# Kernel tuning notes

Hardware: AMD Instinct MI355X
Metric: run time of the kernel (lower is better)

Reference implementation:

```python
import jax, jax.numpy as jnp
import numpy as np

NUM_ITERS = 3  # num_iterations init arg


def squash(t, axis):
    # scale = ||t||^2 / (1+||t||^2); out = scale * t / ||t||
    sn = jnp.sum(t * t, axis=axis, keepdims=True)
    return (sn / (1.0 + sn)) * t / jnp.sqrt(sn)


def setup_inputs() -> dict:
    key = jax.random.key(0)
    k1, k2, k3 = jax.random.split(key, 3)
    B, I, O, DI, DO = 2048, 64, 32, 16, 16
    x = jax.random.normal(k1, (B, DI, I), dtype=jnp.float32)
    route_weights = jax.random.normal(k2, (O, I, DO, DI), dtype=jnp.float32)
    noise = 0.01 * jax.random.normal(k3, (O, I, DO, DI), dtype=jnp.float32)
    return {"x": x, "route_weights": route_weights, "noise": noise}


def reference(x, route_weights, noise):
    # random=True branch: perturbed routing weights
    W = route_weights + noise                      # [O,I,do,di]
    xt = jnp.transpose(x, (0, 2, 1))               # [B,I,di]
    # priors[b,o,i,d] = sum_e W[o,i,d,e] * xt[b,i,e]  (trailing singleton dim dropped)
    priors = jnp.einsum('oide,bie->boid', W, xt)   # [B,O,I,do]
    logits = jnp.zeros_like(priors)
    out = None
    for it in range(NUM_ITERS):
        probs = jax.nn.softmax(logits, axis=2)     # over input capsules I
        out = squash(jnp.sum(probs * priors, axis=2, keepdims=True), axis=3)  # [B,O,1,do]
        if it != NUM_ITERS - 1:
            logits = logits + priors * out         # routing-by-agreement update
    out = out[:, :, 0, :]                          # squeeze -> [B,O,do]
    # unsqueeze(0).transpose(2,1) -> [1,O,B,do]
    return jnp.transpose(out[None], (0, 2, 1, 3))
```

## Files before the change

kernel.cpp:

```cpp
#include <hip/hip_runtime.h>


#define THREADS 512

__global__ __launch_bounds__(THREADS) void routing_kernel(
    const float* __restrict__ x,
    const float* __restrict__ rw,
    const float* __restrict__ ns,
    float* __restrict__ out)
{
    __shared__ float lds[16384];

    const int tid  = threadIdx.x;
    const int w    = tid >> 6;
    const int lane = tid & 63;

    const int o  = blockIdx.x >> 6;
    const int bc = blockIdx.x & 63;
    const int bbase = bc * 32;

    float wq0[16], wq1[16];
    {
        const int base = (o * 64 + lane) * 256 + w * 32;
        #pragma unroll
        for (int eq = 0; eq < 4; ++eq) {
            const float4 a0 = *reinterpret_cast<const float4*>(rw + base + eq * 4);
            const float4 n0 = *reinterpret_cast<const float4*>(ns + base + eq * 4);
            wq0[4*eq+0] = a0.x + n0.x;  wq0[4*eq+1] = a0.y + n0.y;
            wq0[4*eq+2] = a0.z + n0.z;  wq0[4*eq+3] = a0.w + n0.w;
            const float4 a1 = *reinterpret_cast<const float4*>(rw + base + 16 + eq * 4);
            const float4 n1 = *reinterpret_cast<const float4*>(ns + base + 16 + eq * 4);
            wq1[4*eq+0] = a1.x + n1.x;  wq1[4*eq+1] = a1.y + n1.y;
            wq1[4*eq+2] = a1.z + n1.z;  wq1[4*eq+3] = a1.w + n1.w;
        }
    }

    const float* xrd = lds + 8192 + lane;
    const int d0 = 2 * w, d1 = 2 * w + 1;
    const int perm0 = ((((lane >> 2) ^ (d0 & 7)) << 2) | (lane & 3));
    const int perm1 = ((((lane >> 2) ^ (d1 & 7)) << 2) | (lane & 3));
    float* pw0 = lds + d0 * 64 + perm0;
    float* pw1 = lds + d1 * 64 + perm1;

    const int qB  = lane >> 4;
    const int dB  = lane & 15;
    const int swz = dB & 7;
    const float4* prbase = reinterpret_cast<const float4*>(lds) + (w * 16 + dB) * 16;
    const float4* pr0 = prbase + ((4 * qB + 0) ^ swz);
    const float4* pr1 = prbase + ((4 * qB + 1) ^ swz);
    const float4* pr2 = prbase + ((4 * qB + 2) ^ swz);
    const float4* pr3 = prbase + ((4 * qB + 3) ^ swz);

    float4* xwr = reinterpret_cast<float4*>(lds + 8192) + (w * 256 + lane);
    const float4* xsrc0 = reinterpret_cast<const float4*>(x) + bbase * 256
                        + (w * 256 + lane);

    const int outbase = (o * 2048 + bbase + w) * 16 + dB;

    float4 xb0 = xsrc0[0];
    float4 xb1 = xsrc0[64];
    float4 xb2 = xsrc0[128];
    float4 xb3 = xsrc0[192];
    xwr[0] = xb0;  xwr[64] = xb1;  xwr[128] = xb2;  xwr[192] = xb3;
    __syncthreads();

    #pragma unroll
    for (int s = 0; s < 4; ++s) {
        #pragma unroll
        for (int bb = 0; bb < 8; ++bb) {
            float xv[16];
            #pragma unroll
            for (int e = 0; e < 16; ++e)
                xv[e] = xrd[bb * 1024 + e * 64];
            float acc0 = 0.f, acc1 = 0.f;
            #pragma unroll
            for (int e = 0; e < 16; ++e) {
                acc0 = fmaf(wq0[e], xv[e], acc0);
                acc1 = fmaf(wq1[e], xv[e], acc1);
            }
            pw0[bb * 1024] = acc0;
            pw1[bb * 1024] = acc1;
        }
        __syncthreads();

        float p[16];
        {
            const float4 v0 = *pr0, v1 = *pr1, v2 = *pr2, v3 = *pr3;
            p[0]=v0.x; p[1]=v0.y; p[2]=v0.z; p[3]=v0.w;
            p[4]=v1.x; p[5]=v1.y; p[6]=v1.z; p[7]=v1.w;
            p[8]=v2.x; p[9]=v2.y; p[10]=v2.z; p[11]=v2.w;
            p[12]=v3.x; p[13]=v3.y; p[14]=v3.z; p[15]=v3.w;
        }

        if (s < 3) {
            const float4* xsrc = xsrc0 + (s + 1) * 2048;
            xb0 = xsrc[0];  xb1 = xsrc[64];  xb2 = xsrc[128];  xb3 = xsrc[192];
        }

        float t0 = (p[0]+p[1]) + (p[2]+p[3]);
        float t1 = (p[4]+p[5]) + (p[6]+p[7]);
        float t2 = (p[8]+p[9]) + (p[10]+p[11]);
        float t3 = (p[12]+p[13]) + (p[14]+p[15]);
        float part = (t0 + t1) + (t2 + t3);
        part += __shfl_xor(part, 16);
        part += __shfl_xor(part, 32);
        float sv = part * (1.0f / 64.0f);

        float sn = sv * sv;
        sn += __shfl_xor(sn, 1); sn += __shfl_xor(sn, 2);
        sn += __shfl_xor(sn, 4); sn += __shfl_xor(sn, 8);
        float factor = __builtin_amdgcn_sqrtf(sn)
                     * __builtin_amdgcn_rcpf(1.0f + sn);
        float Vsum = sv * factor;

        #pragma unroll
        for (int it = 0; it < 2; ++it) {
            const float c = Vsum * 1.44269504089f;
            float e0, e1, e2, e3;
            float dd0, dd1, dd2, dd3, nn0, nn1, nn2, nn3;
            e0 = __builtin_amdgcn_exp2f(p[0] * c);
            e1 = __builtin_amdgcn_exp2f(p[1] * c);
            e2 = __builtin_amdgcn_exp2f(p[2] * c);
            e3 = __builtin_amdgcn_exp2f(p[3] * c);
            dd0 = e0; dd1 = e1; dd2 = e2; dd3 = e3;
            nn0 = e0 * p[0]; nn1 = e1 * p[1]; nn2 = e2 * p[2]; nn3 = e3 * p[3];
            e0 = __builtin_amdgcn_exp2f(p[4] * c);
            e1 = __builtin_amdgcn_exp2f(p[5] * c);
            e2 = __builtin_amdgcn_exp2f(p[6] * c);
            e3 = __builtin_amdgcn_exp2f(p[7] * c);
            dd0 += e0; dd1 += e1; dd2 += e2; dd3 += e3;
            nn0 = fmaf(e0, p[4], nn0); nn1 = fmaf(e1, p[5], nn1);
            nn2 = fmaf(e2, p[6], nn2); nn3 = fmaf(e3, p[7], nn3);
            e0 = __builtin_amdgcn_exp2f(p[8] * c);
            e1 = __builtin_amdgcn_exp2f(p[9] * c);
            e2 = __builtin_amdgcn_exp2f(p[10] * c);
            e3 = __builtin_amdgcn_exp2f(p[11] * c);
            dd0 += e0; dd1 += e1; dd2 += e2; dd3 += e3;
            nn0 = fmaf(e0, p[8], nn0);  nn1 = fmaf(e1, p[9], nn1);
            nn2 = fmaf(e2, p[10], nn2); nn3 = fmaf(e3, p[11], nn3);
            e0 = __builtin_amdgcn_exp2f(p[12] * c);
            e1 = __builtin_amdgcn_exp2f(p[13] * c);
            e2 = __builtin_amdgcn_exp2f(p[14] * c);
            e3 = __builtin_amdgcn_exp2f(p[15] * c);
            dd0 += e0; dd1 += e1; dd2 += e2; dd3 += e3;
            nn0 = fmaf(e0, p[12], nn0); nn1 = fmaf(e1, p[13], nn1);
            nn2 = fmaf(e2, p[14], nn2); nn3 = fmaf(e3, p[15], nn3);

            float den = (dd0 + dd1) + (dd2 + dd3);
            float num = (nn0 + nn1) + (nn2 + nn3);
            den += __shfl_xor(den, 16); den += __shfl_xor(den, 32);
            num += __shfl_xor(num, 16); num += __shfl_xor(num, 32);
            sv = num * __builtin_amdgcn_rcpf(den);
            sn = sv * sv;
            sn += __shfl_xor(sn, 1); sn += __shfl_xor(sn, 2);
            sn += __shfl_xor(sn, 4); sn += __shfl_xor(sn, 8);
            factor = __builtin_amdgcn_sqrtf(sn)
                   * __builtin_amdgcn_rcpf(1.0f + sn);
            Vsum += sv * factor;
        }

        if (qB == 0)
            out[outbase + s * 128] = sv * factor;

        if (s < 3) {
            xwr[0] = xb0;  xwr[64] = xb1;  xwr[128] = xb2;  xwr[192] = xb3;
        }
        __syncthreads();
    }
}

extern "C" void kernel_launch(void* const* d_in, const int* in_sizes, int n_in,
                              void* d_out, int out_size, void* d_ws, size_t ws_size,
                              hipStream_t stream) {
    const float* x  = (const float*)d_in[0];
    const float* rw = (const float*)d_in[1];
    const float* ns = (const float*)d_in[2];
    float* out = (float*)d_out;
    (void)d_ws; (void)ws_size; (void)in_sizes; (void)n_in; (void)out_size;

    const int grid = 32 * 64;
    routing_kernel<<<grid, THREADS, 0, stream>>>(x, rw, ns, out);
}
```

Measured before the change: 93.39 us.

## Stage x in padded transposed LDS halves and read with float4

The x tile is now staged in two half-batch phases in a transposed, padded LDS layout, so each lane reads its 16 input values with four float4 loads instead of sixteen scalar loads. Shared memory drops from a 64KB static array to about 48.5KB of dynamic LDS, which may let more blocks fit per CU. Global loads for the next half are issued ahead of time and overlap with compute. The cost is extra __syncthreads barriers per stage and more complex index arithmetic.

```diff
diff --git a/kernel.cpp b/kernel.cpp
--- a/kernel.cpp
+++ b/kernel.cpp
@@ -9,7 +9,8 @@
     const float* __restrict__ ns,
     float* __restrict__ out)
 {
-    __shared__ float lds[16384];
+    extern __shared__ float lds[];
+    float* xlds = lds + 8192;
 
     const int tid  = threadIdx.x;
     const int w    = tid >> 6;
@@ -35,12 +36,9 @@
         }
     }
 
-    const float* xrd = lds + 8192 + lane;
     const int d0 = 2 * w, d1 = 2 * w + 1;
-    const int perm0 = ((((lane >> 2) ^ (d0 & 7)) << 2) | (lane & 3));
-    const int perm1 = ((((lane >> 2) ^ (d1 & 7)) << 2) | (lane & 3));
-    float* pw0 = lds + d0 * 64 + perm0;
-    float* pw1 = lds + d1 * 64 + perm1;
+    float* pw0 = lds + d0 * 64 + ((((lane >> 2) ^ (d0 & 7)) << 2) | (lane & 3));
+    float* pw1 = lds + d1 * 64 + ((((lane >> 2) ^ (d1 & 7)) << 2) | (lane & 3));
 
     const int qB  = lane >> 4;
     const int dB  = lane & 15;
@@ -51,36 +49,71 @@
     const float4* pr2 = prbase + ((4 * qB + 2) ^ swz);
     const float4* pr3 = prbase + ((4 * qB + 3) ^ swz);
 
-    float4* xwr = reinterpret_cast<float4*>(lds + 8192) + (w * 256 + lane);
-    const float4* xsrc0 = reinterpret_cast<const float4*>(x) + bbase * 256
-                        + (w * 256 + lane);
+    const float* xrb = xlds + lane * 16 + ((lane >> 3) << 2);
+
+    const int rem = tid & 255;
+    const int b0q = tid >> 8;
+    const int i4  = tid & 15;
+    const int eS  = (tid >> 4) & 15;
+    float* xwA = xlds + b0q * 1056 + i4 * 64 + ((i4 >> 1) << 2) + eS;
+    float* xwB = xwA + 2112;
+    const float4* xsrcB = reinterpret_cast<const float4*>(x) + bbase * 256 + rem;
+    const int gA = b0q * 256;
 
     const int outbase = (o * 2048 + bbase + w) * 16 + dB;
 
-    float4 xb0 = xsrc0[0];
-    float4 xb1 = xsrc0[64];
-    float4 xb2 = xsrc0[128];
-    float4 xb3 = xsrc0[192];
-    xwr[0] = xb0;  xwr[64] = xb1;  xwr[128] = xb2;  xwr[192] = xb3;
+    float4 vA = xsrcB[gA];
+    float4 vB = xsrcB[gA + 512];
+    xwA[0] = vA.x;  xwA[16] = vA.y;  xwA[32] = vA.z;  xwA[48] = vA.w;
+    xwB[0] = vB.x;  xwB[16] = vB.y;  xwB[32] = vB.z;  xwB[48] = vB.w;
+    float4 wA = xsrcB[gA + 1024];
+    float4 wB = xsrcB[gA + 1536];
     __syncthreads();
 
     #pragma unroll
     for (int s = 0; s < 4; ++s) {
-        #pragma unroll
-        for (int bb = 0; bb < 8; ++bb) {
-            float xv[16];
-            #pragma unroll
-            for (int e = 0; e < 16; ++e)
-                xv[e] = xrd[bb * 1024 + e * 64];
-            float acc0 = 0.f, acc1 = 0.f;
-            #pragma unroll
-            for (int e = 0; e < 16; ++e) {
-                acc0 = fmaf(wq0[e], xv[e], acc0);
-                acc1 = fmaf(wq1[e], xv[e], acc1);
-            }
-            pw0[bb * 1024] = acc0;
-            pw1[bb * 1024] = acc1;
-        }
+        #define APHASE(H)                                                        \
+        {                                                                        \
+            _Pragma("unroll")                                                    \
+            for (int bb = 0; bb < 4; ++bb) {                                     \
+                const float4 v0 = *reinterpret_cast<const float4*>(xrb + bb * 1056 + 0);  \
+                const float4 v1 = *reinterpret_cast<const float4*>(xrb + bb * 1056 + 4);  \
+                const float4 v2 = *reinterpret_cast<const float4*>(xrb + bb * 1056 + 8);  \
+                const float4 v3 = *reinterpret_cast<const float4*>(xrb + bb * 1056 + 12); \
+                float a0 = 0.f, a1 = 0.f;                                        \
+                a0 = fmaf(wq0[0],  v0.x, a0);  a1 = fmaf(wq1[0],  v0.x, a1);     \
+                a0 = fmaf(wq0[1],  v0.y, a0);  a1 = fmaf(wq1[1],  v0.y, a1);     \
+                a0 = fmaf(wq0[2],  v0.z, a0);  a1 = fmaf(wq1[2],  v0.z, a1);     \
+                a0 = fmaf(wq0[3],  v0.w, a0);  a1 = fmaf(wq1[3],  v0.w, a1);     \
+                a0 = fmaf(wq0[4],  v1.x, a0);  a1 = fmaf(wq1[4],  v1.x, a1);     \
+                a0 = fmaf(wq0[5],  v1.y, a0);  a1 = fmaf(wq1[5],  v1.y, a1);     \
+                a0 = fmaf(wq0[6],  v1.z, a0);  a1 = fmaf(wq1[6],  v1.z, a1);     \
+                a0 = fmaf(wq0[7],  v1.w, a0);  a1 = fmaf(wq1[7],  v1.w, a1);     \
+                a0 = fmaf(wq0[8],  v2.x, a0);  a1 = fmaf(wq1[8],  v2.x, a1);     \
+                a0 = fmaf(wq0[9],  v2.y, a0);  a1 = fmaf(wq1[9],  v2.y, a1);     \
+                a0 = fmaf(wq0[10], v2.z, a0);  a1 = fmaf(wq1[10], v2.z, a1);     \
+                a0 = fmaf(wq0[11], v2.w, a0);  a1 = fmaf(wq1[11], v2.w, a1);     \
+                a0 = fmaf(wq0[12], v3.x, a0);  a1 = fmaf(wq1[12], v3.x, a1);     \
+                a0 = fmaf(wq0[13], v3.y, a0);  a1 = fmaf(wq1[13], v3.y, a1);     \
+                a0 = fmaf(wq0[14], v3.z, a0);  a1 = fmaf(wq1[14], v3.z, a1);     \
+                a0 = fmaf(wq0[15], v3.w, a0);  a1 = fmaf(wq1[15], v3.w, a1);     \
+                pw0[((H) * 4 + bb) * 1024] = a0;                                 \
+                pw1[((H) * 4 + bb) * 1024] = a1;                                 \
+            }                                                                    \
+        }
+
+        APHASE(0)
+        __syncthreads();
+
+        xwA[0] = wA.x;  xwA[16] = wA.y;  xwA[32] = wA.z;  xwA[48] = wA.w;
+        xwB[0] = wB.x;  xwB[16] = wB.y;  xwB[32] = wB.z;  xwB[48] = wB.w;
+        if (s < 3) {
+            vA = xsrcB[gA + (s + 1) * 2048];
+            vB = xsrcB[gA + (s + 1) * 2048 + 512];
+        }
+        __syncthreads();
+
+        APHASE(1)
         __syncthreads();
 
         float p[16];
@@ -93,8 +126,10 @@
         }
 
         if (s < 3) {
-            const float4* xsrc = xsrc0 + (s + 1) * 2048;
-            xb0 = xsrc[0];  xb1 = xsrc[64];  xb2 = xsrc[128];  xb3 = xsrc[192];
+            xwA[0] = vA.x;  xwA[16] = vA.y;  xwA[32] = vA.z;  xwA[48] = vA.w;
+            xwB[0] = vB.x;  xwB[16] = vB.y;  xwB[32] = vB.z;  xwB[48] = vB.w;
+            wA = xsrcB[gA + (s + 1) * 2048 + 1024];
+            wB = xsrcB[gA + (s + 1) * 2048 + 1536];
         }
 
         float t0 = (p[0]+p[1]) + (p[2]+p[3]);
@@ -162,9 +197,6 @@
         if (qB == 0)
             out[outbase + s * 128] = sv * factor;
 
-        if (s < 3) {
-            xwr[0] = xb0;  xwr[64] = xb1;  xwr[128] = xb2;  xwr[192] = xb3;
-        }
         __syncthreads();
     }
 }
@@ -179,5 +211,5 @@
     (void)d_ws; (void)ws_size; (void)in_sizes; (void)n_in; (void)out_size;
 
     const int grid = 32 * 64;
-    routing_kernel<<<grid, THREADS, 0, stream>>>(x, rw, ns, out);
+    routing_kernel<<<grid, THREADS, 49664, stream>>>(x, rw, ns, out);
 }
```

After: 83.79 us. -10.3%, faster.
